# Performance work log

Hardware: AMD Instinct MI355X
Metric: run time of the kernel (lower is better)

Reference implementation:

```python
import jax, jax.numpy as jnp
import numpy as np

SAMPLE_THRESH = 0.05  # self.sample_thresh


def grid_sample_bilinear_zeros(img, pts):
    """torch.nn.functional.grid_sample with mode='bilinear', align_corners=False,
    padding_mode='zeros'. img: [C, H, W]; pts: [N, 2] with (x, y) in [-1, 1].
    Returns [C, N]."""
    C, H, W = img.shape
    # align_corners=False unnormalization
    x = (pts[:, 0] + 1.0) * (W / 2.0) - 0.5
    y = (pts[:, 1] + 1.0) * (H / 2.0) - 0.5
    x0 = jnp.floor(x)
    y0 = jnp.floor(y)
    wx1 = x - x0
    wy1 = y - y0
    wx0 = 1.0 - wx1
    wy0 = 1.0 - wy1

    def gather(xi, yi):
        valid = (xi >= 0) & (xi < W) & (yi >= 0) & (yi < H)
        xi_c = jnp.clip(xi, 0, W - 1).astype(jnp.int32)
        yi_c = jnp.clip(yi, 0, H - 1).astype(jnp.int32)
        v = img[:, yi_c, xi_c]  # [C, N]
        return v * valid.astype(img.dtype)[None, :]

    out = (gather(x0, y0) * (wx0 * wy0)[None, :]
           + gather(x0 + 1, y0) * (wx1 * wy0)[None, :]
           + gather(x0, y0 + 1) * (wx0 * wy1)[None, :]
           + gather(x0 + 1, y0 + 1) * (wx1 * wy1)[None, :])
    return out


def setup_inputs() -> dict:
    key = jax.random.key(0)
    k1, k2, k3, k4 = jax.random.split(key, 4)
    N_A, N_B = 8192, 8192
    H, W2 = 504, 1008  # warp is [hs, 2*ws, 4] per post_process
    x_A = jax.random.uniform(k1, (N_A, 2), jnp.float32, -1.0, 1.0)
    x_B = jax.random.uniform(k2, (N_B, 2), jnp.float32, -1.0, 1.0)
    warp = jax.random.uniform(k3, (H, W2, 4), jnp.float32, -1.0, 1.0)
    certainty = jax.random.uniform(k4, (H, W2), jnp.float32, 0.0, 1.0)
    return {"x_A": x_A, "x_B": x_B, "warp": warp, "certainty": certainty}


def reference(x_A, x_B, warp, certainty):
    # --- match_keypoints ---
    # x_A_to_B = grid_sample(warp[..., -2:].permute(2,0,1)[None], x_A[None,None])[0,:,0].mT
    flow_img = jnp.transpose(warp[..., -2:], (2, 0, 1))  # [2, H, 2W]
    x_A_to_B = grid_sample_bilinear_zeros(flow_img, x_A).T  # [N_A, 2]
    cert_A_to_B = grid_sample_bilinear_zeros(certainty[None], x_A)[0]  # [N_A]

    # D = torch.cdist(x_A_to_B, x_B) via |a|^2 + |b|^2 - 2 a.b
    a2 = jnp.sum(x_A_to_B * x_A_to_B, axis=-1)  # [N_A]
    b2 = jnp.sum(x_B * x_B, axis=-1)            # [N_B]
    D2 = a2[:, None] + b2[None, :] - 2.0 * (x_A_to_B @ x_B.T)
    D = jnp.sqrt(jnp.maximum(D2, 1e-12))  # [N_A, N_B]

    # mutual nearest-neighbor mask with certainty threshold
    row_min = jnp.min(D, axis=-1, keepdims=True)
    col_min = jnp.min(D, axis=-2, keepdims=True)
    mask = (D == row_min) & (D == col_min) & (cert_A_to_B[:, None] > SAMPLE_THRESH)

    # jit-compatible equivalent of torch.nonzero: distances at mutual-NN pairs,
    # zero elsewhere. nonzero entries == matched (inds_A, inds_B) pairs.
    return jnp.where(mask, D, 0.0)
```

## Files before the change

kernel.cpp:

```cpp
#include <hip/hip_runtime.h>
#include <math.h>

#define SAMPLE_THRESH 0.05f

__device__ __forceinline__ float d2_exact(float xa0, float xa1, float a2,
                                          float xb0, float xb1, float b2) {
    float p  = __fmul_rn(xa1, xb1);
    float q  = __fmaf_rn(xa0, xb0, p);
    float s  = __fadd_rn(a2, b2);
    return __fmaf_rn(-2.0f, q, s);
}

__device__ __forceinline__ float D_from_d2(float d2) {
    return __fsqrt_rn(fmaxf(d2, 1e-12f));
}

__global__ __launch_bounds__(256) void sample_kernel(
    const float* __restrict__ xA, const float* __restrict__ xB,
    const float4* __restrict__ warp, const float* __restrict__ cert,
    float4* __restrict__ Apack, float4* __restrict__ Bpack,
    int nA, int nB, int H, int W) {
    int i = blockIdx.x * blockDim.x + threadIdx.x;
    if (i < nA) {
        float px = xA[2 * i + 0], py = xA[2 * i + 1];
        float xf = (px + 1.0f) * (0.5f * (float)W) - 0.5f;
        float yf = (py + 1.0f) * (0.5f * (float)H) - 0.5f;
        float x0f = floorf(xf), y0f = floorf(yf);
        float wx1 = xf - x0f, wy1 = yf - y0f;
        float wx0 = 1.0f - wx1, wy0 = 1.0f - wy1;
        int x0 = (int)x0f, y0 = (int)y0f;
        float fx = 0.0f, fy = 0.0f, cv = 0.0f;
#pragma unroll
        for (int dy = 0; dy < 2; ++dy) {
#pragma unroll
            for (int dx = 0; dx < 2; ++dx) {
                int xi = x0 + dx, yi = y0 + dy;
                float vm = (xi >= 0 && xi < W && yi >= 0 && yi < H) ? 1.0f : 0.0f;
                int xc = min(max(xi, 0), W - 1);
                int yc = min(max(yi, 0), H - 1);
                int idx = yc * W + xc;
                float4 wv = warp[idx];
                float  c  = cert[idx];
                float wgt = (dx ? wx1 : wx0) * (dy ? wy1 : wy0);
                fx += (wv.z * vm) * wgt;
                fy += (wv.w * vm) * wgt;
                cv += (c    * vm) * wgt;
            }
        }
        float a2 = fx * fx + fy * fy;
        Apack[i] = make_float4(fx, fy, a2, cv);
    }
    if (i < nB) {
        float b0 = xB[2 * i + 0], b1 = xB[2 * i + 1];
        Bpack[i] = make_float4(b0, b1, b0 * b0 + b1 * b1, 0.0f);
    }
}

__global__ __launch_bounds__(256) void min_kernel(
    const float4* __restrict__ Apack, const float4* __restrict__ Bpack,
    float4* __restrict__ rowpack, float4* __restrict__ colpack,
    int nA, int nB) {
    int gwave = (int)((blockIdx.x * blockDim.x + threadIdx.x) >> 6);
    int lane = threadIdx.x & 63;
    int nRowWaves = nA / 4;
    float m0 = 1e30f, m1 = 1e30f, m2 = 1e30f, m3 = 1e30f;
    if (gwave < nRowWaves) {
        int i0 = gwave * 4;
        float4 A0 = Apack[i0 + 0], A1 = Apack[i0 + 1];
        float4 A2 = Apack[i0 + 2], A3 = Apack[i0 + 3];
        for (int j = lane; j < nB; j += 64) {
            float4 b = Bpack[j];
            m0 = fminf(m0, d2_exact(A0.x, A0.y, A0.z, b.x, b.y, b.z));
            m1 = fminf(m1, d2_exact(A1.x, A1.y, A1.z, b.x, b.y, b.z));
            m2 = fminf(m2, d2_exact(A2.x, A2.y, A2.z, b.x, b.y, b.z));
            m3 = fminf(m3, d2_exact(A3.x, A3.y, A3.z, b.x, b.y, b.z));
        }
#pragma unroll
        for (int o = 32; o; o >>= 1) {
            m0 = fminf(m0, __shfl_xor(m0, o, 64));
            m1 = fminf(m1, __shfl_xor(m1, o, 64));
            m2 = fminf(m2, __shfl_xor(m2, o, 64));
            m3 = fminf(m3, __shfl_xor(m3, o, 64));
        }
        if (lane == 0) {
            rowpack[i0 + 0] = make_float4(A0.x, A0.y, A0.z, (A0.w > SAMPLE_THRESH) ? D_from_d2(m0) : -1.0f);
            rowpack[i0 + 1] = make_float4(A1.x, A1.y, A1.z, (A1.w > SAMPLE_THRESH) ? D_from_d2(m1) : -1.0f);
            rowpack[i0 + 2] = make_float4(A2.x, A2.y, A2.z, (A2.w > SAMPLE_THRESH) ? D_from_d2(m2) : -1.0f);
            rowpack[i0 + 3] = make_float4(A3.x, A3.y, A3.z, (A3.w > SAMPLE_THRESH) ? D_from_d2(m3) : -1.0f);
        }
    } else {
        int j0 = (gwave - nRowWaves) * 4;
        if (j0 >= nB) return;
        float4 B0 = Bpack[j0 + 0], B1 = Bpack[j0 + 1];
        float4 B2 = Bpack[j0 + 2], B3 = Bpack[j0 + 3];
        for (int i = lane; i < nA; i += 64) {
            float4 a = Apack[i];
            m0 = fminf(m0, d2_exact(a.x, a.y, a.z, B0.x, B0.y, B0.z));
            m1 = fminf(m1, d2_exact(a.x, a.y, a.z, B1.x, B1.y, B1.z));
            m2 = fminf(m2, d2_exact(a.x, a.y, a.z, B2.x, B2.y, B2.z));
            m3 = fminf(m3, d2_exact(a.x, a.y, a.z, B3.x, B3.y, B3.z));
        }
#pragma unroll
        for (int o = 32; o; o >>= 1) {
            m0 = fminf(m0, __shfl_xor(m0, o, 64));
            m1 = fminf(m1, __shfl_xor(m1, o, 64));
            m2 = fminf(m2, __shfl_xor(m2, o, 64));
            m3 = fminf(m3, __shfl_xor(m3, o, 64));
        }
        if (lane == 0) {
            colpack[j0 + 0] = make_float4(B0.x, B0.y, B0.z, D_from_d2(m0));
            colpack[j0 + 1] = make_float4(B1.x, B1.y, B1.z, D_from_d2(m1));
            colpack[j0 + 2] = make_float4(B2.x, B2.y, B2.z, D_from_d2(m2));
            colpack[j0 + 3] = make_float4(B3.x, B3.y, B3.z, D_from_d2(m3));
        }
    }
}

#define TI 64
#define TJ 1024
__global__ __launch_bounds__(256) void out_kernel(
    const float4* __restrict__ rowpack, const float4* __restrict__ colpack,
    float* __restrict__ out, int N) {
    __shared__ float4 cp[TJ];
    __shared__ float4 rp[TI];
    int tid = threadIdx.x;
    int j0 = blockIdx.x * TJ;
    int i0 = blockIdx.y * TI;
    for (int k = tid; k < TJ; k += 256) cp[k] = colpack[j0 + k];
    if (tid < TI) rp[tid] = rowpack[i0 + tid];
    __syncthreads();
    float4 c0 = cp[tid * 4 + 0], c1 = cp[tid * 4 + 1];
    float4 c2 = cp[tid * 4 + 2], c3 = cp[tid * 4 + 3];
    size_t base = (size_t)i0 * (size_t)N + (size_t)j0 + (size_t)tid * 4;
    for (int r = 0; r < TI; ++r) {
        float4 a = rp[r];
        float d0 = D_from_d2(d2_exact(a.x, a.y, a.z, c0.x, c0.y, c0.z));
        float d1 = D_from_d2(d2_exact(a.x, a.y, a.z, c1.x, c1.y, c1.z));
        float d2 = D_from_d2(d2_exact(a.x, a.y, a.z, c2.x, c2.y, c2.z));
        float d3 = D_from_d2(d2_exact(a.x, a.y, a.z, c3.x, c3.y, c3.z));
        float4 o;
        o.x = (d0 == a.w && d0 == c0.w) ? d0 : 0.0f;
        o.y = (d1 == a.w && d1 == c1.w) ? d1 : 0.0f;
        o.z = (d2 == a.w && d2 == c2.w) ? d2 : 0.0f;
        o.w = (d3 == a.w && d3 == c3.w) ? d3 : 0.0f;
        *(float4*)(out + base + (size_t)r * (size_t)N) = o;
    }
}

extern "C" void kernel_launch(void* const* d_in, const int* in_sizes, int n_in,
                              void* d_out, int out_size, void* d_ws, size_t ws_size,
                              hipStream_t stream) {
    const float* xA   = (const float*)d_in[0];
    const float* xB   = (const float*)d_in[1];
    const float* warp = (const float*)d_in[2];
    const float* cert = (const float*)d_in[3];
    int nA = in_sizes[0] / 2;
    int nB = in_sizes[1] / 2;
    const int H = 504, W = 1008;
    float* out = (float*)d_out;

    char* ws = (char*)d_ws;
    float4* Apack   = (float4*)ws;
    float4* Bpack   = Apack + nA;
    float4* rowpack = Bpack + nB;
    float4* colpack = rowpack + nA;

    int nmax = nA > nB ? nA : nB;
    sample_kernel<<<(nmax + 255) / 256, 256, 0, stream>>>(
        xA, xB, (const float4*)warp, cert, Apack, Bpack, nA, nB, H, W);

    int totWaves = nA / 4 + nB / 4;
    min_kernel<<<(totWaves * 64 + 255) / 256, 256, 0, stream>>>(
        Apack, Bpack, rowpack, colpack, nA, nB);

    dim3 grid(nB / TJ, nA / TI);
    out_kernel<<<grid, 256, 0, stream>>>(rowpack, colpack, out, nB);
}
```

Measured before the change: 325.3 us.

## Compare squared distances against precomputed sqrt-preimage thresholds and use nontemporal stores

The min kernel now computes, for each row and column minimum, the largest squared distance whose rounded sqrt equals the minimum distance. This lets the output kernel compare raw squared distances against thresholds instead of taking a sqrt per element, and it writes the precomputed row distance directly. The min kernel processes 8 rows or columns per wave instead of 4, and output stores become nontemporal. The threshold search adds a small serial loop per row and column, and it relies on sqrt being monotone so that masks stay bit-exact.

```diff
diff --git a/kernel.cpp b/kernel.cpp
--- a/kernel.cpp
+++ b/kernel.cpp
@@ -2,6 +2,8 @@
 #include <math.h>
 
 #define SAMPLE_THRESH 0.05f
+
+typedef float f32x4 __attribute__((ext_vector_type(4)));
 
 __device__ __forceinline__ float d2_exact(float xa0, float xa1, float a2,
                                           float xb0, float xb1, float b2) {
@@ -11,8 +13,23 @@
     return __fmaf_rn(-2.0f, q, s);
 }
 
-__device__ __forceinline__ float D_from_d2(float d2) {
+__device__ __forceinline__ float f_D(float d2) {
     return __fsqrt_rn(fmaxf(d2, 1e-12f));
+}
+
+__device__ __forceinline__ float nextf_pos(float x) {
+    return __int_as_float(__float_as_int(x) + 1);
+}
+__device__ __forceinline__ float prevf_pos(float x) {
+    return __int_as_float(__float_as_int(x) - 1);
+}
+
+__device__ __forceinline__ float hi_thresh(float m) {
+    float t = f_D(m);
+    float x = fmaxf(m, __fmul_rn(t, t));
+    while (f_D(x) > t) x = prevf_pos(x);
+    while (f_D(nextf_pos(x)) <= t) x = nextf_pos(x);
+    return x;
 }
 
 __global__ __launch_bounds__(256) void sample_kernel(
@@ -58,60 +75,76 @@
 
 __global__ __launch_bounds__(256) void min_kernel(
     const float4* __restrict__ Apack, const float4* __restrict__ Bpack,
-    float4* __restrict__ rowpack, float4* __restrict__ colpack,
-    int nA, int nB) {
+    float4* __restrict__ rowpack, float* __restrict__ rowD,
+    float4* __restrict__ colpack, int nA, int nB) {
     int gwave = (int)((blockIdx.x * blockDim.x + threadIdx.x) >> 6);
     int lane = threadIdx.x & 63;
-    int nRowWaves = nA / 4;
+    int nRowWaves = nA / 8;
     float m0 = 1e30f, m1 = 1e30f, m2 = 1e30f, m3 = 1e30f;
+    float m4 = 1e30f, m5 = 1e30f, m6 = 1e30f, m7 = 1e30f;
     if (gwave < nRowWaves) {
-        int i0 = gwave * 4;
-        float4 A0 = Apack[i0 + 0], A1 = Apack[i0 + 1];
-        float4 A2 = Apack[i0 + 2], A3 = Apack[i0 + 3];
+        int i0 = gwave * 8;
+        float4 A0 = Apack[i0 + 0], A1 = Apack[i0 + 1], A2 = Apack[i0 + 2], A3 = Apack[i0 + 3];
+        float4 A4 = Apack[i0 + 4], A5 = Apack[i0 + 5], A6 = Apack[i0 + 6], A7 = Apack[i0 + 7];
         for (int j = lane; j < nB; j += 64) {
             float4 b = Bpack[j];
             m0 = fminf(m0, d2_exact(A0.x, A0.y, A0.z, b.x, b.y, b.z));
             m1 = fminf(m1, d2_exact(A1.x, A1.y, A1.z, b.x, b.y, b.z));
             m2 = fminf(m2, d2_exact(A2.x, A2.y, A2.z, b.x, b.y, b.z));
             m3 = fminf(m3, d2_exact(A3.x, A3.y, A3.z, b.x, b.y, b.z));
+            m4 = fminf(m4, d2_exact(A4.x, A4.y, A4.z, b.x, b.y, b.z));
+            m5 = fminf(m5, d2_exact(A5.x, A5.y, A5.z, b.x, b.y, b.z));
+            m6 = fminf(m6, d2_exact(A6.x, A6.y, A6.z, b.x, b.y, b.z));
+            m7 = fminf(m7, d2_exact(A7.x, A7.y, A7.z, b.x, b.y, b.z));
         }
 #pragma unroll
         for (int o = 32; o; o >>= 1) {
-            m0 = fminf(m0, __shfl_xor(m0, o, 64));
-            m1 = fminf(m1, __shfl_xor(m1, o, 64));
-            m2 = fminf(m2, __shfl_xor(m2, o, 64));
-            m3 = fminf(m3, __shfl_xor(m3, o, 64));
+            m0 = fminf(m0, __shfl_xor(m0, o, 64)); m1 = fminf(m1, __shfl_xor(m1, o, 64));
+            m2 = fminf(m2, __shfl_xor(m2, o, 64)); m3 = fminf(m3, __shfl_xor(m3, o, 64));
+            m4 = fminf(m4, __shfl_xor(m4, o, 64)); m5 = fminf(m5, __shfl_xor(m5, o, 64));
+            m6 = fminf(m6, __shfl_xor(m6, o, 64)); m7 = fminf(m7, __shfl_xor(m7, o, 64));
         }
         if (lane == 0) {
-            rowpack[i0 + 0] = make_float4(A0.x, A0.y, A0.z, (A0.w > SAMPLE_THRESH) ? D_from_d2(m0) : -1.0f);
-            rowpack[i0 + 1] = make_float4(A1.x, A1.y, A1.z, (A1.w > SAMPLE_THRESH) ? D_from_d2(m1) : -1.0f);
-            rowpack[i0 + 2] = make_float4(A2.x, A2.y, A2.z, (A2.w > SAMPLE_THRESH) ? D_from_d2(m2) : -1.0f);
-            rowpack[i0 + 3] = make_float4(A3.x, A3.y, A3.z, (A3.w > SAMPLE_THRESH) ? D_from_d2(m3) : -1.0f);
+#define ROW_OUT(K, AK, MK)                                                         \
+            {                                                                      \
+                float Dm = f_D(MK);                                                \
+                float hi = (AK.w > SAMPLE_THRESH) ? hi_thresh(MK) : -1e30f;        \
+                rowpack[i0 + K] = make_float4(AK.x, AK.y, AK.z, hi);               \
+                rowD[i0 + K] = Dm;                                                 \
+            }
+            ROW_OUT(0, A0, m0) ROW_OUT(1, A1, m1) ROW_OUT(2, A2, m2) ROW_OUT(3, A3, m3)
+            ROW_OUT(4, A4, m4) ROW_OUT(5, A5, m5) ROW_OUT(6, A6, m6) ROW_OUT(7, A7, m7)
+#undef ROW_OUT
         }
     } else {
-        int j0 = (gwave - nRowWaves) * 4;
+        int j0 = (gwave - nRowWaves) * 8;
         if (j0 >= nB) return;
-        float4 B0 = Bpack[j0 + 0], B1 = Bpack[j0 + 1];
-        float4 B2 = Bpack[j0 + 2], B3 = Bpack[j0 + 3];
+        float4 B0 = Bpack[j0 + 0], B1 = Bpack[j0 + 1], B2 = Bpack[j0 + 2], B3 = Bpack[j0 + 3];
+        float4 B4 = Bpack[j0 + 4], B5 = Bpack[j0 + 5], B6 = Bpack[j0 + 6], B7 = Bpack[j0 + 7];
         for (int i = lane; i < nA; i += 64) {
             float4 a = Apack[i];
             m0 = fminf(m0, d2_exact(a.x, a.y, a.z, B0.x, B0.y, B0.z));
             m1 = fminf(m1, d2_exact(a.x, a.y, a.z, B1.x, B1.y, B1.z));
             m2 = fminf(m2, d2_exact(a.x, a.y, a.z, B2.x, B2.y, B2.z));
             m3 = fminf(m3, d2_exact(a.x, a.y, a.z, B3.x, B3.y, B3.z));
+            m4 = fminf(m4, d2_exact(a.x, a.y, a.z, B4.x, B4.y, B4.z));
+            m5 = fminf(m5, d2_exact(a.x, a.y, a.z, B5.x, B5.y, B5.z));
+            m6 = fminf(m6, d2_exact(a.x, a.y, a.z, B6.x, B6.y, B6.z));
+            m7 = fminf(m7, d2_exact(a.x, a.y, a.z, B7.x, B7.y, B7.z));
         }
 #pragma unroll
         for (int o = 32; o; o >>= 1) {
-            m0 = fminf(m0, __shfl_xor(m0, o, 64));
-            m1 = fminf(m1, __shfl_xor(m1, o, 64));
-            m2 = fminf(m2, __shfl_xor(m2, o, 64));
-            m3 = fminf(m3, __shfl_xor(m3, o, 64));
+            m0 = fminf(m0, __shfl_xor(m0, o, 64)); m1 = fminf(m1, __shfl_xor(m1, o, 64));
+            m2 = fminf(m2, __shfl_xor(m2, o, 64)); m3 = fminf(m3, __shfl_xor(m3, o, 64));
+            m4 = fminf(m4, __shfl_xor(m4, o, 64)); m5 = fminf(m5, __shfl_xor(m5, o, 64));
+            m6 = fminf(m6, __shfl_xor(m6, o, 64)); m7 = fminf(m7, __shfl_xor(m7, o, 64));
         }
         if (lane == 0) {
-            colpack[j0 + 0] = make_float4(B0.x, B0.y, B0.z, D_from_d2(m0));
-            colpack[j0 + 1] = make_float4(B1.x, B1.y, B1.z, D_from_d2(m1));
-            colpack[j0 + 2] = make_float4(B2.x, B2.y, B2.z, D_from_d2(m2));
-            colpack[j0 + 3] = make_float4(B3.x, B3.y, B3.z, D_from_d2(m3));
+#define COL_OUT(K, BK, MK)                                                         \
+            colpack[j0 + K] = make_float4(BK.x, BK.y, BK.z, hi_thresh(MK));
+            COL_OUT(0, B0, m0) COL_OUT(1, B1, m1) COL_OUT(2, B2, m2) COL_OUT(3, B3, m3)
+            COL_OUT(4, B4, m4) COL_OUT(5, B5, m5) COL_OUT(6, B6, m6) COL_OUT(7, B7, m7)
+#undef COL_OUT
         }
     }
 }
@@ -119,31 +152,34 @@
 #define TI 64
 #define TJ 1024
 __global__ __launch_bounds__(256) void out_kernel(
-    const float4* __restrict__ rowpack, const float4* __restrict__ colpack,
-    float* __restrict__ out, int N) {
+    const float4* __restrict__ rowpack, const float* __restrict__ rowD,
+    const float4* __restrict__ colpack, float* __restrict__ out, int N) {
     __shared__ float4 cp[TJ];
     __shared__ float4 rp[TI];
+    __shared__ float rd[TI];
     int tid = threadIdx.x;
     int j0 = blockIdx.x * TJ;
     int i0 = blockIdx.y * TI;
     for (int k = tid; k < TJ; k += 256) cp[k] = colpack[j0 + k];
-    if (tid < TI) rp[tid] = rowpack[i0 + tid];
+    if (tid < TI) { rp[tid] = rowpack[i0 + tid]; rd[tid] = rowD[i0 + tid]; }
     __syncthreads();
     float4 c0 = cp[tid * 4 + 0], c1 = cp[tid * 4 + 1];
     float4 c2 = cp[tid * 4 + 2], c3 = cp[tid * 4 + 3];
     size_t base = (size_t)i0 * (size_t)N + (size_t)j0 + (size_t)tid * 4;
+#pragma unroll 2
     for (int r = 0; r < TI; ++r) {
         float4 a = rp[r];
-        float d0 = D_from_d2(d2_exact(a.x, a.y, a.z, c0.x, c0.y, c0.z));
-        float d1 = D_from_d2(d2_exact(a.x, a.y, a.z, c1.x, c1.y, c1.z));
-        float d2 = D_from_d2(d2_exact(a.x, a.y, a.z, c2.x, c2.y, c2.z));
-        float d3 = D_from_d2(d2_exact(a.x, a.y, a.z, c3.x, c3.y, c3.z));
-        float4 o;
-        o.x = (d0 == a.w && d0 == c0.w) ? d0 : 0.0f;
-        o.y = (d1 == a.w && d1 == c1.w) ? d1 : 0.0f;
-        o.z = (d2 == a.w && d2 == c2.w) ? d2 : 0.0f;
-        o.w = (d3 == a.w && d3 == c3.w) ? d3 : 0.0f;
-        *(float4*)(out + base + (size_t)r * (size_t)N) = o;
+        float Dm = rd[r];
+        float d0 = d2_exact(a.x, a.y, a.z, c0.x, c0.y, c0.z);
+        float d1 = d2_exact(a.x, a.y, a.z, c1.x, c1.y, c1.z);
+        float d2 = d2_exact(a.x, a.y, a.z, c2.x, c2.y, c2.z);
+        float d3 = d2_exact(a.x, a.y, a.z, c3.x, c3.y, c3.z);
+        f32x4 o;
+        o.x = (d0 <= a.w && d0 <= c0.w) ? Dm : 0.0f;
+        o.y = (d1 <= a.w && d1 <= c1.w) ? Dm : 0.0f;
+        o.z = (d2 <= a.w && d2 <= c2.w) ? Dm : 0.0f;
+        o.w = (d3 <= a.w && d3 <= c3.w) ? Dm : 0.0f;
+        __builtin_nontemporal_store(o, (f32x4*)(out + base + (size_t)r * (size_t)N));
     }
 }
 
@@ -164,15 +200,16 @@
     float4* Bpack   = Apack + nA;
     float4* rowpack = Bpack + nB;
     float4* colpack = rowpack + nA;
+    float*  rowD    = (float*)(colpack + nB);
 
     int nmax = nA > nB ? nA : nB;
     sample_kernel<<<(nmax + 255) / 256, 256, 0, stream>>>(
         xA, xB, (const float4*)warp, cert, Apack, Bpack, nA, nB, H, W);
 
-    int totWaves = nA / 4 + nB / 4;
+    int totWaves = nA / 8 + nB / 8;
     min_kernel<<<(totWaves * 64 + 255) / 256, 256, 0, stream>>>(
-        Apack, Bpack, rowpack, colpack, nA, nB);
+        Apack, Bpack, rowpack, rowD, colpack, nA, nB);
 
     dim3 grid(nB / TJ, nA / TI);
-    out_kernel<<<grid, 256, 0, stream>>>(rowpack, colpack, out, nB);
-}
+    out_kernel<<<grid, 256, 0, stream>>>(rowpack, rowD, colpack, out, nB);
+}
```

Result: no change. 330.8 us (+1.7%).
